# Kernel tuning notes

Hardware: AMD Instinct MI355X
Metric: run time of the kernel (lower is better)

## Reference

```python
import jax, jax.numpy as jnp
import numpy as np

# Dimensions (production-scale, see shape_source)
B, L, D = 16, 64, 256      # batch, text length, char_emb
U = 500                    # number of distinct units (characters/phonemes)
V = 10000                  # vocab size
MIN_WL, MAX_WL = 4, 10     # min/max extracted word length
WL = MAX_WL - MIN_WL + 1   # number of candidate word lengths (7)
TEMP = 0.1                 # g.temperature
INS_COST = 1.0             # per-character insertion/deletion cost


def setup_inputs() -> dict:
    key = jax.random.key(0)
    k1, k2, k3, k4 = jax.random.split(key, 4)
    word_repr = jax.random.normal(k1, (B, L, D), jnp.float32)
    unit_repr = jax.random.normal(k2, (U, D), jnp.float32)
    indexed_segments = jax.random.randint(k3, (V, MAX_WL), 0, U)
    vocab_length = jax.random.randint(k4, (V,), MIN_WL, MAX_WL + 1)
    return {
        "word_repr": word_repr,
        "unit_repr": unit_repr,
        "indexed_segments": indexed_segments,
        "vocab_length": vocab_length,
    }


def _soft_max(x, axis):
    w = jnp.exp(jax.nn.log_softmax(x / TEMP, axis=axis))
    value = (x * w).sum(axis)
    index = jnp.argmax(x, axis=axis)
    return value, index


def _soft_min(x, axis):
    w = jnp.exp(jax.nn.log_softmax(-x / TEMP, axis=axis))
    value = (x * w).sum(axis)
    index = jnp.argmin(x, axis=axis)
    return value, index


def _soft_threshold(x):
    return (jax.nn.celu(1.0 - 2.0 * x) + 1.0) / 2.0


def reference(word_repr, unit_repr, indexed_segments, vocab_length):
    # --- cosine char-similarity between text positions and vocab units ---
    wn = word_repr / jnp.linalg.norm(word_repr, axis=-1, keepdims=True)   # (B,L,D)
    un = unit_repr / jnp.linalg.norm(unit_repr, axis=-1, keepdims=True)   # (U,D)
    sim = jnp.einsum('bld,ud->blu', wn, un)                               # (B,L,U)
    # pad along length so s+j gathers are in-range; padded dist is masked later
    simp = jnp.pad(sim, ((0, 0), (0, MAX_WL), (0, 0)))                    # (B,L+ML,U)

    wls = jnp.arange(MIN_WL, MAX_WL + 1)                                  # (WL,)

    # --- aligned edit-distance accumulation d(v, w) over char positions ---
    # ed[b,s,k,v] = sum_{j < min(wl_k, len_v)} (1 - cos(text[b,s+j], vocab_char[v,j]))
    ed = jnp.zeros((B, L, WL, V), jnp.float32)
    for j in range(MAX_WL):
        d_j = 1.0 - simp[:, j:j + L, :][:, :, indexed_segments[:, j]]     # (B,L,V)
        m_j = (j < jnp.minimum(wls[:, None], vocab_length[None, :]))      # (WL,V)
        ed = ed + d_j[:, :, None, :] * m_j.astype(jnp.float32)[None, None]
    # length-mismatch penalty (insert/delete)
    ed = ed + INS_COST * jnp.abs(wls[:, None] - vocab_length[None, :]).astype(jnp.float32)

    # --- soft-min over vocab: matched_ed_dist / matched_vocab ---
    matched_ed, matched_vocab = _soft_min(ed, axis=-1)                    # (B,L,WL)
    matched_length = vocab_length[matched_vocab]                          # (B,L,WL)
    # soft threshold on per-character distance, then score = thresh * |w|
    matched_thresh = _soft_threshold(matched_ed / wls.astype(jnp.float32))
    matched_score = matched_thresh * wls.astype(jnp.float32)              # (B,L,WL)

    # --- viability and scatter restore into dense (batch, len_s, len_e) ---
    s_idx = jnp.arange(L)[:, None]                                        # (L,1)
    viable = (s_idx + wls[None, :]) <= L                                  # (L,WL)
    score = jnp.where(viable[None], matched_score, 0.0)                   # (B,L,WL)
    e_idx = jnp.clip(s_idx + wls[None, :] - 1, 0, L - 1)                  # (L,WL)
    s_grid = jnp.broadcast_to(s_idx, (L, WL))
    dense = jnp.zeros((B, L, L), jnp.float32).at[:, s_grid, e_idx].add(
        score * viable[None].astype(jnp.float32))                         # (B,len_s,len_e)

    # --- soft-max over all candidate spans ---
    flat = dense.reshape(B, L * L)
    best_score, best_idx = _soft_max(flat, axis=-1)                       # (B,)
    start = best_idx // L
    end = best_idx % L
    wl_sel = jnp.clip(end - start + 1 - MIN_WL, 0, WL - 1)
    best_vocab = matched_vocab[jnp.arange(B), start, wl_sel]              # (B,)

    return start, end, best_score, best_vocab, dense
```

## Files before the change

### kernel.cpp

```cpp
#include <hip/hip_runtime.h>

#define NB 16
#define NL 64
#define ND 256
#define NU 500
#define NV 10000
#define MINWL 4
#define MAXWL 10
#define NWL 7
#define ITEMP 10.0f
#define L2I 14.4269504088896f
#define NT 512
#define NTX 1024
#define NWAVES 16
#define NCH 16
#define RSTR 501
#define DLPAD 32568
#define SEGL_SLOTS 648
#define EXT_LDS_BYTES ((DLPAD + SEGL_SLOTS * 8) * 4)
#define NSK (NWL * 64)
#define NZERO 3690.0f

__global__ __launch_bounds__(512) void k_sort(const int* __restrict__ vlen,
                                              int* __restrict__ origv,
                                              int* __restrict__ bases) {
    int t = threadIdx.x;
    int lv[20];
    if (t < 500) {
        const int4* vp = (const int4*)(vlen + t * 20);
        int4 q0 = vp[0], q1 = vp[1], q2 = vp[2], q3 = vp[3], q4 = vp[4];
        int raw[20] = {q0.x, q0.y, q0.z, q0.w, q1.x, q1.y, q1.z, q1.w,
                       q2.x, q2.y, q2.z, q2.w, q3.x, q3.y, q3.z, q3.w,
                       q4.x, q4.y, q4.z, q4.w};
#pragma unroll
        for (int j = 0; j < 20; ++j) lv[j] = raw[j] - MINWL;
    } else {
#pragma unroll
        for (int j = 0; j < 20; ++j) lv[j] = -1;
    }
    unsigned long long hA = 0, hB = 0;
#pragma unroll
    for (int j = 0; j < 20; ++j) {
        int l = lv[j];
        if (l >= 0) {
            int sh = (l & 3) * 16;
            unsigned long long inc = 1ULL << sh;
            bool isA = l < 4;
            hA += isA ? inc : 0ULL;
            hB += isA ? 0ULL : inc;
        }
    }
    int lane = t & 63, wv = t >> 6;
    unsigned long long iA = hA, iB = hB;
#pragma unroll
    for (int o = 1; o < 64; o <<= 1) {
        unsigned long long a2 = (unsigned long long)__shfl_up((long long)iA, o);
        unsigned long long b2 = (unsigned long long)__shfl_up((long long)iB, o);
        if (lane >= o) { iA += a2; iB += b2; }
    }
    __shared__ unsigned long long wA[8], wB[8];
    __shared__ int base_s[8];
    if (lane == 63) { wA[wv] = iA; wB[wv] = iB; }
    __syncthreads();
    unsigned long long pA = 0, pB = 0, tA = 0, tB = 0;
#pragma unroll
    for (int w2 = 0; w2 < 8; ++w2) {
        if (w2 < wv) { pA += wA[w2]; pB += wB[w2]; }
        tA += wA[w2]; tB += wB[w2];
    }
    unsigned long long eA = pA + iA - hA, eB = pB + iB - hB;
    if (t == 0) {
        int tot[7] = {(int)(tA & 0xFFFF), (int)((tA >> 16) & 0xFFFF),
                      (int)((tA >> 32) & 0xFFFF), (int)((tA >> 48) & 0xFFFF),
                      (int)(tB & 0xFFFF), (int)((tB >> 16) & 0xFFFF),
                      (int)((tB >> 32) & 0xFFFF)};
        int run = 0;
        for (int l = 0; l < 7; ++l) { base_s[l] = run; bases[l] = run; run += tot[l]; }
        base_s[7] = run; bases[7] = run;
    }
    __syncthreads();
    unsigned long long qA = eA + ((unsigned long long)base_s[0] |
                                  ((unsigned long long)base_s[1] << 16) |
                                  ((unsigned long long)base_s[2] << 32) |
                                  ((unsigned long long)base_s[3] << 48));
    unsigned long long qB = eB + ((unsigned long long)base_s[4] |
                                  ((unsigned long long)base_s[5] << 16) |
                                  ((unsigned long long)base_s[6] << 32));
#pragma unroll
    for (int j = 0; j < 20; ++j) {
        int l = lv[j];
        if (l >= 0) {
            int sh = (l & 3) * 16;
            bool isA = l < 4;
            unsigned long long cur = isA ? qA : qB;
            int pos = (int)((cur >> sh) & 0xFFFF);
            origv[pos] = t * 20 + j;
            unsigned long long inc = 1ULL << sh;
            qA += isA ? inc : 0ULL;
            qB += isA ? 0ULL : inc;
        }
    }
}

#define SSTR 260
#define SIM_LDS_BYTES ((2 * 32 * SSTR + 64) * 4)

__global__ __launch_bounds__(256) void k_simgather(const float* __restrict__ word,
                                                   const float* __restrict__ unit,
                                                   float* __restrict__ sim,
                                                   const int* __restrict__ origv,
                                                   const int* __restrict__ seg,
                                                   unsigned int* __restrict__ segP) {
    int blk = blockIdx.x;
    int t = threadIdx.x;
    if (blk >= 512) {
        int i = (blk - 512) * 256 + t;
        if (i < NV) {
            int v = origv[i];
            const int2* sp = (const int2*)(seg + v * MAXWL);
            int2 a0 = sp[0], a1 = sp[1], a2 = sp[2], a3 = sp[3], a4 = sp[4];
            unsigned int* dst = segP + i * 8;
            *(uint4*)dst = make_uint4((unsigned)(a0.x | (a0.y << 16)),
                                      (unsigned)(a1.x | (a1.y << 16)),
                                      (unsigned)(a2.x | (a2.y << 16)),
                                      (unsigned)(a3.x | (a3.y << 16)));
            dst[4] = (unsigned)(a4.x | (a4.y << 16));
        }
        return;
    }
    extern __shared__ float lds[];
    float* wt = lds;
    float* ut = lds + 32 * SSTR;
    float* scaleW = lds + 64 * SSTR;
    float* scaleU = scaleW + 32;
    int uc = blk & 15, lt = (blk >> 4) & 1, b = blk >> 5;
    int l0 = lt * 32, u0 = uc * 32;

#pragma unroll
    for (int i = 0; i < 32; ++i)
        wt[i * SSTR + t] = word[(b * NL + l0 + i) * ND + t];
#pragma unroll
    for (int i = 0; i < 32; ++i) {
        int u = u0 + i;
        ut[i * SSTR + t] = (u < NU) ? unit[u * ND + t] : 1.0f;
    }
    __syncthreads();
#pragma unroll
    for (int h = 0; h < 2; ++h) {
        int r = (t >> 4) + h * 16, p = t & 15;
        float sw = 0.f, su = 0.f;
#pragma unroll
        for (int c = 0; c < 16; ++c) {
            float x = wt[r * SSTR + p * 16 + c];
            float y = ut[r * SSTR + p * 16 + c];
            sw += x * x; su += y * y;
        }
#pragma unroll
        for (int o = 1; o < 16; o <<= 1) {
            sw += __shfl_xor(sw, o);
            su += __shfl_xor(su, o);
        }
        if (p == 0) { scaleW[r] = 1.0f / sqrtf(sw); scaleU[r] = 1.0f / sqrtf(su); }
    }
    __syncthreads();

    int lane = t & 15;
    int lp = t >> 4;
    int l = lp * 2;
    const float4* w0p = (const float4*)(wt + l * SSTR);
    const float4* w1p = (const float4*)(wt + (l + 1) * SSTR);
    const float4* x0p = (const float4*)(ut + lane * SSTR);
    const float4* x1p = (const float4*)(ut + (lane + 16) * SSTR);
    float a00 = 0.f, a01 = 0.f, a10 = 0.f, a11 = 0.f;
#pragma unroll 8
    for (int dq = 0; dq < ND / 4; ++dq) {
        float4 w0 = w0p[dq], w1 = w1p[dq], x0 = x0p[dq], x1 = x1p[dq];
        a00 += w0.x * x0.x + w0.y * x0.y + w0.z * x0.z + w0.w * x0.w;
        a01 += w0.x * x1.x + w0.y * x1.y + w0.z * x1.z + w0.w * x1.w;
        a10 += w1.x * x0.x + w1.y * x0.y + w1.z * x0.z + w1.w * x0.w;
        a11 += w1.x * x1.x + w1.y * x1.y + w1.z * x1.z + w1.w * x1.w;
    }
    float sw0 = scaleW[l], sw1 = scaleW[l + 1];
    float su0 = scaleU[lane], su1 = scaleU[lane + 16];
    int gu0 = u0 + lane, gu1 = u0 + lane + 16;
    int base = (b * NL + l0 + l) * NU;
    if (gu0 < NU) { sim[base + gu0] = a00 * (sw0 * su0); sim[base + NU + gu0] = a10 * (sw1 * su0); }
    if (gu1 < NU) { sim[base + gu1] = a01 * (sw0 * su1); sim[base + NU + gu1] = a11 * (sw1 * su1); }
}


template <int L>
__device__ __forceinline__ void item_compute(unsigned p0, unsigned p1, unsigned p2,
                                             unsigned p3, unsigned p4, int li,
                                             const float* __restrict__ dl,
                                             const int* __restrict__ rowoff,
                                             float& Sb, float& Wb, float& mb, int& ixb,
                                             float& Sm, float& Wm, float& mmv, int& ixm) {
    unsigned c[10];
    c[0] = p0 & 0xFFFF; c[1] = p0 >> 16;
    c[2] = p1 & 0xFFFF; c[3] = p1 >> 16;
    c[4] = p2 & 0xFFFF; c[5] = p2 >> 16;
    c[6] = p3 & 0xFFFF; c[7] = p3 >> 16;
    c[8] = p4 & 0xFFFF; c[9] = p4 >> 16;
    float q = ((dl[rowoff[0] + c[0]] + dl[rowoff[1] + c[1]]) +
               dl[rowoff[2] + c[2]]) + dl[rowoff[3] + c[3]];
    float pm = q;
#pragma unroll
    for (int j = 4; j < L; ++j) {
        if (j == L - 1) pm = q;
        q += dl[rowoff[j] + c[j]];
    }
    float wb = __builtin_amdgcn_exp2f(fmaf(q, -L2I, (float)L * L2I));
    Sb += wb;
    Wb = fmaf(q, wb, Wb);
    bool lb = q < mb;
    ixb = lb ? li : ixb;
    mb = lb ? q : mb;
    if constexpr (L >= 5) {
        float edm = pm + 1.0f;
        float wm = __builtin_amdgcn_exp2f(fmaf(edm, -L2I, (float)(L - 1) * L2I));
        Sm += wm;
        Wm = fmaf(edm, wm, Wm);
        bool lm = edm < mmv;
        ixm = lm ? li : ixm;
        mmv = lm ? edm : mmv;
    }
}

template <int L>
__device__ __forceinline__ void bucket_passL(int a, int e, int gofs,
                                             const unsigned int* __restrict__ segL,
                                             const float* __restrict__ dl,
                                             const int* __restrict__ rowoff,
                                             float* m, float* S, float* W, int* ix) {
    if (a >= e) return;
    float Sb = 0.f, Wb = 0.f, mb = 3.0e38f;
    float Sm = 0.f, Wm = 0.f, mmv = 3.0e38f;
    int ixb = 0, ixm = 0;

    unsigned a0, a1, a2, a3, a4, b0, b1, b2, b3, b4;
    {
        const uint4 pv = *(const uint4*)(segL + a * 8);
        a0 = pv.x; a1 = pv.y; a2 = pv.z; a3 = pv.w;
        a4 = (L > 8) ? segL[a * 8 + 4] : 0u;
        int i1 = min(a + 1, e - 1);
        const uint4 qv = *(const uint4*)(segL + i1 * 8);
        b0 = qv.x; b1 = qv.y; b2 = qv.z; b3 = qv.w;
        b4 = (L > 8) ? segL[i1 * 8 + 4] : 0u;
    }
    for (int li = a; li < e; li += 2) {
        int n0i = min(li + 2, e - 1), n1i = min(li + 3, e - 1);
        const uint4 nv = *(const uint4*)(segL + n0i * 8);
        unsigned n00 = nv.x, n01 = nv.y, n02 = nv.z, n03 = nv.w;
        unsigned n04 = (L > 8) ? segL[n0i * 8 + 4] : 0u;
        const uint4 mv2 = *(const uint4*)(segL + n1i * 8);
        unsigned n10 = mv2.x, n11 = mv2.y, n12 = mv2.z, n13 = mv2.w;
        unsigned n14 = (L > 8) ? segL[n1i * 8 + 4] : 0u;

        item_compute<L>(a0, a1, a2, a3, a4, li, dl, rowoff,
                        Sb, Wb, mb, ixb, Sm, Wm, mmv, ixm);
        if (li + 1 < e)
            item_compute<L>(b0, b1, b2, b3, b4, li + 1, dl, rowoff,
                            Sb, Wb, mb, ixb, Sm, Wm, mmv, ixm);

        a0 = n00; a1 = n01; a2 = n02; a3 = n03; a4 = n04;
        b0 = n10; b1 = n11; b2 = n12; b3 = n13; b4 = n14;
    }

    int gb = ixb + gofs, gm_ = ixm + gofs;
#pragma unroll
    for (int k = 0; k < NWL; ++k) {
        if (k >= L - 4) {
            float c = (float)(k + 4 - L);
            S[k] += Sb;
            W[k] += fmaf(c, Sb, Wb);
            float cand = mb + c;
            bool take = (cand < m[k]) || (cand == m[k] && gb < ix[k]);
            ix[k] = take ? gb : ix[k];
            m[k] = take ? cand : m[k];
        }
        if constexpr (L >= 5) {
            if (k == L - 5) {
                S[k] += Sm;
                W[k] += Wm;
                bool take = (mmv < m[k]) || (mmv == m[k] && gm_ < ix[k]);
                ix[k] = take ? gm_ : ix[k];
                m[k] = take ? mmv : m[k];
            }
        }
    }
}

__global__ __launch_bounds__(NTX, 1) void k_extract(const float* __restrict__ sim,
                                                    const unsigned int* __restrict__ segP,
                                                    const int* __restrict__ basesG,
                                                    float* __restrict__ pM,
                                                    float* __restrict__ pS,
                                                    float* __restrict__ pW,
                                                    int* __restrict__ pI) {
    extern __shared__ float dl[];
    unsigned int* segL = (unsigned int*)(dl + DLPAD);
    int blk = blockIdx.x;
    int ch = blk & (NCH - 1), b = blk >> 4;
    int t = threadIdx.x;
    int s = t & 63, w = t >> 6;

    int cs[7], ne[7], lb[7];
    {
        int run = 0;
#pragma unroll
        for (int l = 0; l < 7; ++l) {
            int lo = basesG[l], hi = basesG[l + 1];
            int n = hi - lo;
            int pc = (n + NCH - 1) >> 4;
            int c0 = lo + ch * pc;
            int c1 = min(c0 + pc, hi);
            cs[l] = c0;
            ne[l] = max(c1 - c0, 0);
            lb[l] = run;
            run += ne[l];
        }
    }

    {
        const float2* simq = (const float2*)(sim + b * NL * NU);
        for (int idx = t; idx < NL * 250; idx += NTX) {
            int r = idx / 250;
            int u2 = idx - r * 250;
            float2 g = simq[idx];
            float* ds = dl + r * RSTR + u2 * 2;
            ds[0] = 1.0f - g.x;
            ds[1] = 1.0f - g.y;
        }
        if (t < NU + 1) dl[64 * RSTR + t] = 0.0f;
    }
#pragma unroll
    for (int l = 0; l < 7; ++l) {
        for (int ii = t; ii < ne[l]; ii += NTX) {
            const unsigned int* gp = segP + (cs[l] + ii) * 8;
            uint4 pv = *(const uint4*)gp;
            unsigned int w4 = gp[4];
            unsigned int* dp = segL + (lb[l] + ii) * 8;
            *(uint4*)dp = pv;
            dp[4] = w4;
        }
    }
    __syncthreads();

    int rowoff[10];
#pragma unroll
    for (int j = 0; j < 10; ++j) rowoff[j] = min(s + j, 64) * RSTR;

    float m[NWL], S[NWL], W[NWL];
    int ix[NWL];
#pragma unroll
    for (int k = 0; k < NWL; ++k) { m[k] = 3.0e38f; S[k] = 0.f; W[k] = 0.f; ix[k] = 0; }

    int la[7], le[7];
#pragma unroll
    for (int l = 0; l < 7; ++l) {
        int pw = (ne[l] + NWAVES - 1) >> 4;
        la[l] = lb[l] + w * pw;
        le[l] = min(la[l] + pw, lb[l] + ne[l]);
    }
    bucket_passL<4>(la[0], le[0], cs[0] - lb[0], segL, dl, rowoff, m, S, W, ix);
    bucket_passL<5>(la[1], le[1], cs[1] - lb[1], segL, dl, rowoff, m, S, W, ix);
    bucket_passL<6>(la[2], le[2], cs[2] - lb[2], segL, dl, rowoff, m, S, W, ix);
    bucket_passL<7>(la[3], le[3], cs[3] - lb[3], segL, dl, rowoff, m, S, W, ix);
    bucket_passL<8>(la[4], le[4], cs[4] - lb[4], segL, dl, rowoff, m, S, W, ix);
    bucket_passL<9>(la[5], le[5], cs[5] - lb[5], segL, dl, rowoff, m, S, W, ix);
    bucket_passL<10>(la[6], le[6], cs[6] - lb[6], segL, dl, rowoff, m, S, W, ix);

    __syncthreads();
    float* scrM = dl;
    float* scrS = dl + NWAVES * NSK;
    float* scrW = dl + 2 * NWAVES * NSK;
    int* scrI = (int*)(dl + 3 * NWAVES * NSK);
#pragma unroll
    for (int k = 0; k < NWL; ++k) {
        int o = (w * NWL + k) * 64 + s;
        scrM[o] = m[k]; scrS[o] = S[k]; scrW[o] = W[k]; scrI[o] = ix[k];
    }
    __syncthreads();
    if (t < NSK) {
        int k = t >> 6, ss = t & 63;
        int o0 = k * 64 + ss;
        float mm = scrM[o0], SS = scrS[o0], WW = scrW[o0];
        int II = scrI[o0];
#pragma unroll
        for (int w2 = 1; w2 < NWAVES; ++w2) {
            int o = (w2 * NWL + k) * 64 + ss;
            float m2 = scrM[o];
            int i2 = scrI[o];
            bool take = (m2 < mm) || (m2 == mm && i2 < II);
            II = take ? i2 : II;
            mm = take ? m2 : mm;
            SS += scrS[o];
            WW += scrW[o];
        }
        int off = (b * NCH + ch) * NSK + t;
        pM[off] = mm; pS[off] = SS; pW[off] = WW; pI[off] = II;
    }
}

__global__ __launch_bounds__(NT) void k_merge(const float* __restrict__ pM,
                                              const float* __restrict__ pS,
                                              const float* __restrict__ pW,
                                              const int* __restrict__ pI,
                                              const int* __restrict__ origv,
                                              float* __restrict__ out) {
    int b = blockIdx.x, t = threadIdx.x;
    __shared__ float score[NSK];
    __shared__ int ixf[NSK];
    __shared__ float rm[8], rS[8], rW[8];
    __shared__ int rX[8];
    __shared__ float gm;
    __shared__ int gfl;

    float x = -1.0f;
    int fl = 0x7FFFFFFF;
    if (t < NSK) {
        int base = b * NCH * NSK + t;
        float mm = pM[base], SS = pS[base], WW = pW[base];
        int II = pI[base];
        for (int c = 1; c < NCH; ++c) {
            int o = base + c * NSK;
            float m2 = pM[o];
            int i2 = pI[o];
            bool take = (m2 < mm) || (m2 == mm && i2 < II);
            II = take ? i2 : II;
            mm = take ? m2 : mm;
            SS += pS[o];
            WW += pW[o];
        }
        int k = t >> 6, ss = t & 63;
        int kmax = min(NWL - 1, 60 - ss);
        if (k <= kmax) {
            float med = WW / SS;
            float wl = (float)(MINWL + k);
            float z = 1.0f - 2.0f * (med / wl);
            float cel = (z > 0.f) ? z : (__expf(z) - 1.0f);
            x = 0.5f * (cel + 1.0f) * wl;
            ixf[t] = II;
            fl = ss * 64 + (ss + k + 3);
        }
        score[t] = (k <= kmax) ? x : 0.0f;
    }
    __syncthreads();

    float mv = x;
    int mf = fl;
#pragma unroll
    for (int o = 32; o >= 1; o >>= 1) {
        float m2 = __shfl_down(mv, o);
        int f2 = __shfl_down(mf, o);
        bool take = (m2 > mv) || (m2 == mv && f2 < mf);
        mv = take ? m2 : mv;
        mf = take ? f2 : mf;
    }
    if ((t & 63) == 0) { rm[t >> 6] = mv; rX[t >> 6] = mf; }
    __syncthreads();
    if (t == 0) {
        float mm = rm[0];
        int ff = rX[0];
#pragma unroll
        for (int w2 = 1; w2 < 8; ++w2) {
            bool take = (rm[w2] > mm) || (rm[w2] == mm && rX[w2] < ff);
            mm = take ? rm[w2] : mm;
            ff = take ? rX[w2] : ff;
        }
        gm = mm; gfl = ff;
    }
    __syncthreads();
    float M = gm;

    float Sl = 0.f, Wl = 0.f;
    if (x >= 0.0f) {
        float wq = __expf((x - M) * ITEMP);
        Sl = wq;
        Wl = x * wq;
    }
#pragma unroll
    for (int o = 32; o >= 1; o >>= 1) {
        Sl += __shfl_down(Sl, o);
        Wl += __shfl_down(Wl, o);
    }
    if ((t & 63) == 0) { rS[t >> 6] = Sl; rW[t >> 6] = Wl; }
    __syncthreads();
    if (t == 0) {
        float SS = 0.f, WW = 0.f;
#pragma unroll
        for (int w2 = 0; w2 < 8; ++w2) { SS += rS[w2]; WW += rW[w2]; }
        SS += NZERO * __expf(-M * ITEMP);
        float best = WW / SS;
        int st = gfl >> 6, en = gfl & 63;
        int ks = en - st - 3;
        int II = ixf[ks * 64 + st];
        out[b] = (float)st;
        out[NB + b] = (float)en;
        out[2 * NB + b] = best;
        out[3 * NB + b] = (float)origv[II];
    }

    float* dense = out + 4 * NB + b * NL * NL;
    for (int f = t; f < NL * NL; f += NT) {
        int ss = f >> 6, ee = f & 63;
        int k = ee - ss - 3;
        dense[f] = (k >= 0 && k < NWL) ? score[k * 64 + ss] : 0.0f;
    }
}

extern "C" void kernel_launch(void* const* d_in, const int* in_sizes, int n_in,
                              void* d_out, int out_size, void* d_ws, size_t ws_size,
                              hipStream_t stream) {
    const float* word = (const float*)d_in[0];
    const float* unit = (const float*)d_in[1];
    const int* seg = (const int*)d_in[2];
    const int* vlen = (const int*)d_in[3];
    float* out = (float*)d_out;
    char* ws = (char*)d_ws;
    float* sim = (float*)ws;
    int* origv = (int*)(ws + 2048000);
    int* bases = (int*)(ws + 2088000);
    unsigned int* segP = (unsigned int*)(ws + 2088032);
    float* pM = (float*)(ws + 2408032);
    float* pS = (float*)(ws + 2866784);
    float* pW = (float*)(ws + 3325536);
    int* pI = (int*)(ws + 3784288);

    hipFuncSetAttribute((const void*)k_simgather,
                        hipFuncAttributeMaxDynamicSharedMemorySize, SIM_LDS_BYTES);
    hipFuncSetAttribute((const void*)k_extract,
                        hipFuncAttributeMaxDynamicSharedMemorySize, EXT_LDS_BYTES);

    k_sort<<<1, 512, 0, stream>>>(vlen, origv, bases);
    k_simgather<<<512 + 40, 256, SIM_LDS_BYTES, stream>>>(word, unit, sim,
                                                          origv, seg, segP);
    k_extract<<<NB * NCH, NTX, EXT_LDS_BYTES, stream>>>(sim, segP, bases, pM, pS, pW, pI);
    k_merge<<<NB, NT, 0, stream>>>(pM, pS, pW, pI, origv, out);
}
```

Measured before the change: 61.46 us.

## Fuse merge kernel into extract via last-block atomic counter

Removes the separate k_merge launch. Each extract block increments a per-batch atomic counter, and the last of the 16 chunk blocks for that batch does the merge, softmax and dense write, reusing dynamic LDS. This saves a kernel launch and its dependency gap, but adds a memset launch and a serialized tail in which one block per batch does the merge. Correctness depends on the threadfence plus acquire-release ordering making the other blocks' partial results visible to the last block.

```diff
diff --git a/kernel.cpp b/kernel.cpp
--- a/kernel.cpp
+++ b/kernel.cpp
@@ -10,7 +10,6 @@
 #define NWL 7
 #define ITEMP 10.0f
 #define L2I 14.4269504088896f
-#define NT 512
 #define NTX 1024
 #define NWAVES 16
 #define NCH 16
@@ -294,10 +293,13 @@
 __global__ __launch_bounds__(NTX, 1) void k_extract(const float* __restrict__ sim,
                                                     const unsigned int* __restrict__ segP,
                                                     const int* __restrict__ basesG,
+                                                    const int* __restrict__ origv,
                                                     float* __restrict__ pM,
                                                     float* __restrict__ pS,
                                                     float* __restrict__ pW,
-                                                    int* __restrict__ pI) {
+                                                    int* __restrict__ pI,
+                                                    unsigned int* __restrict__ cnt,
+                                                    float* __restrict__ out) {
     extern __shared__ float dl[];
     unsigned int* segL = (unsigned int*)(dl + DLPAD);
     int blk = blockIdx.x;
@@ -401,19 +403,24 @@
         int off = (b * NCH + ch) * NSK + t;
         pM[off] = mm; pS[off] = SS; pW[off] = WW; pI[off] = II;
     }
-}
-
-__global__ __launch_bounds__(NT) void k_merge(const float* __restrict__ pM,
-                                              const float* __restrict__ pS,
-                                              const float* __restrict__ pW,
-                                              const int* __restrict__ pI,
-                                              const int* __restrict__ origv,
-                                              float* __restrict__ out) {
-    int b = blockIdx.x, t = threadIdx.x;
-    __shared__ float score[NSK];
-    __shared__ int ixf[NSK];
-    __shared__ float rm[8], rS[8], rW[8];
-    __shared__ int rX[8];
+
+    __syncthreads();
+    __shared__ int lastFlag;
+    if (t == 0) {
+        __threadfence();
+        unsigned prev = __hip_atomic_fetch_add(&cnt[b], 1u, __ATOMIC_ACQ_REL,
+                                               __HIP_MEMORY_SCOPE_AGENT);
+        lastFlag = (prev == NCH - 1);
+    }
+    __syncthreads();
+    if (!lastFlag) return;
+
+    float* score = dl;
+    int* ixf = (int*)(dl + NSK);
+    float* rm = dl + 2 * NSK;
+    float* rS = rm + 16;
+    float* rW = rS + 16;
+    int* rX = (int*)(rW + 16);
     __shared__ float gm;
     __shared__ int gfl;
 
@@ -458,13 +465,13 @@
         mv = take ? m2 : mv;
         mf = take ? f2 : mf;
     }
-    if ((t & 63) == 0) { rm[t >> 6] = mv; rX[t >> 6] = mf; }
+    if ((t & 63) == 0) { rm[w] = mv; rX[w] = mf; }
     __syncthreads();
     if (t == 0) {
         float mm = rm[0];
         int ff = rX[0];
 #pragma unroll
-        for (int w2 = 1; w2 < 8; ++w2) {
+        for (int w2 = 1; w2 < NWAVES; ++w2) {
             bool take = (rm[w2] > mm) || (rm[w2] == mm && rX[w2] < ff);
             mm = take ? rm[w2] : mm;
             ff = take ? rX[w2] : ff;
@@ -485,12 +492,12 @@
         Sl += __shfl_down(Sl, o);
         Wl += __shfl_down(Wl, o);
     }
-    if ((t & 63) == 0) { rS[t >> 6] = Sl; rW[t >> 6] = Wl; }
+    if ((t & 63) == 0) { rS[w] = Sl; rW[w] = Wl; }
     __syncthreads();
     if (t == 0) {
         float SS = 0.f, WW = 0.f;
 #pragma unroll
-        for (int w2 = 0; w2 < 8; ++w2) { SS += rS[w2]; WW += rW[w2]; }
+        for (int w2 = 0; w2 < NWAVES; ++w2) { SS += rS[w2]; WW += rW[w2]; }
         SS += NZERO * __expf(-M * ITEMP);
         float best = WW / SS;
         int st = gfl >> 6, en = gfl & 63;
@@ -503,7 +510,7 @@
     }
 
     float* dense = out + 4 * NB + b * NL * NL;
-    for (int f = t; f < NL * NL; f += NT) {
+    for (int f = t; f < NL * NL; f += NTX) {
         int ss = f >> 6, ee = f & 63;
         int k = ee - ss - 3;
         dense[f] = (k >= 0 && k < NWL) ? score[k * 64 + ss] : 0.0f;
@@ -527,15 +534,17 @@
     float* pS = (float*)(ws + 2866784);
     float* pW = (float*)(ws + 3325536);
     int* pI = (int*)(ws + 3784288);
+    unsigned int* cnt = (unsigned int*)(ws + 4243040);
 
     hipFuncSetAttribute((const void*)k_simgather,
                         hipFuncAttributeMaxDynamicSharedMemorySize, SIM_LDS_BYTES);
     hipFuncSetAttribute((const void*)k_extract,
                         hipFuncAttributeMaxDynamicSharedMemorySize, EXT_LDS_BYTES);
 
+    hipMemsetAsync(cnt, 0, NB * sizeof(unsigned int), stream);
     k_sort<<<1, 512, 0, stream>>>(vlen, origv, bases);
     k_simgather<<<512 + 40, 256, SIM_LDS_BYTES, stream>>>(word, unit, sim,
                                                           origv, seg, segP);
-    k_extract<<<NB * NCH, NTX, EXT_LDS_BYTES, stream>>>(sim, segP, bases, pM, pS, pW, pI);
-    k_merge<<<NB, NT, 0, stream>>>(pM, pS, pW, pI, origv, out);
+    k_extract<<<NB * NCH, NTX, EXT_LDS_BYTES, stream>>>(sim, segP, bases, origv,
+                                                        pM, pS, pW, pI, cnt, out);
 }
```

Result: slower. 95.54 us, median of 2 (+55.4%).

## Assign waves to length buckets by weighted cost instead of splitting every bucket

Applied to the files above, without the earlier changes.

Replaces the scheme where each of the 16 waves walks a slice of all seven length buckets with one where each wave owns a single bucket. Waves are apportioned greedily by bucket size times a length-dependent cost weight. Each wave then runs one specialised bucket pass chosen by a switch, which removes the per-bucket loop overhead and uneven tail slices. The risks are load imbalance from the coarse per-bucket apportioning and divergence from the runtime switch across templated passes.

```diff
diff --git a/kernel.cpp b/kernel.cpp
--- a/kernel.cpp
+++ b/kernel.cpp
@@ -356,20 +356,50 @@
 #pragma unroll
     for (int k = 0; k < NWL; ++k) { m[k] = 3.0e38f; S[k] = 0.f; W[k] = 0.f; ix[k] = 0; }
 
-    int la[7], le[7];
-#pragma unroll
-    for (int l = 0; l < 7; ++l) {
-        int pw = (ne[l] + NWAVES - 1) >> 4;
-        la[l] = lb[l] + w * pw;
-        le[l] = min(la[l] + pw, lb[l] + ne[l]);
-    }
-    bucket_passL<4>(la[0], le[0], cs[0] - lb[0], segL, dl, rowoff, m, S, W, ix);
-    bucket_passL<5>(la[1], le[1], cs[1] - lb[1], segL, dl, rowoff, m, S, W, ix);
-    bucket_passL<6>(la[2], le[2], cs[2] - lb[2], segL, dl, rowoff, m, S, W, ix);
-    bucket_passL<7>(la[3], le[3], cs[3] - lb[3], segL, dl, rowoff, m, S, W, ix);
-    bucket_passL<8>(la[4], le[4], cs[4] - lb[4], segL, dl, rowoff, m, S, W, ix);
-    bucket_passL<9>(la[5], le[5], cs[5] - lb[5], segL, dl, rowoff, m, S, W, ix);
-    bucket_passL<10>(la[6], le[6], cs[6] - lb[6], segL, dl, rowoff, m, S, W, ix);
+    int nw[7];
+    {
+        int used = 0;
+#pragma unroll
+        for (int l = 0; l < 7; ++l) { nw[l] = (ne[l] > 0) ? 1 : 0; used += nw[l]; }
+        if (used == 0) { nw[0] = NWAVES; used = NWAVES; }
+        for (int r = used; r < NWAVES; ++r) {
+            int best = 0;
+            long bc = -1;
+#pragma unroll
+            for (int l = 0; l < 7; ++l) {
+                if (nw[l] > 0) {
+                    long c = (long)ne[l] * (l + 7) / nw[l];
+                    if (c > bc) { bc = c; best = l; }
+                }
+            }
+            nw[best]++;
+        }
+    }
+    int myl = 0, wi = 0;
+    {
+        int acc = 0;
+#pragma unroll
+        for (int l = 0; l < 7; ++l) {
+            bool in = (w >= acc) && (w < acc + nw[l]);
+            myl = in ? l : myl;
+            wi = in ? (w - acc) : wi;
+            acc += nw[l];
+        }
+    }
+    int nwl = nw[myl];
+    int pw = (ne[myl] + nwl - 1) / nwl;
+    int a = lb[myl] + wi * pw;
+    int e = min(a + pw, lb[myl] + ne[myl]);
+    int go = cs[myl] - lb[myl];
+    switch (myl) {
+        case 0: bucket_passL<4>(a, e, go, segL, dl, rowoff, m, S, W, ix); break;
+        case 1: bucket_passL<5>(a, e, go, segL, dl, rowoff, m, S, W, ix); break;
+        case 2: bucket_passL<6>(a, e, go, segL, dl, rowoff, m, S, W, ix); break;
+        case 3: bucket_passL<7>(a, e, go, segL, dl, rowoff, m, S, W, ix); break;
+        case 4: bucket_passL<8>(a, e, go, segL, dl, rowoff, m, S, W, ix); break;
+        case 5: bucket_passL<9>(a, e, go, segL, dl, rowoff, m, S, W, ix); break;
+        case 6: bucket_passL<10>(a, e, go, segL, dl, rowoff, m, S, W, ix); break;
+    }
 
     __syncthreads();
     float* scrM = dl;
```

After: 71.63 us. +16.5%, slower.
